# Optimization experiments

Measured on AMD Instinct MI355X. Metric: run time of the kernel, lower is better.

The kernel has to match this reference:

```python
import jax, jax.numpy as jnp
import numpy as np

T, B, E, H = 2048, 2, 1024, 16
HD = E // H
NEG = -1e9  # large negative for causal additive mask


def setup_inputs() -> dict:
    key = jax.random.key(0)
    ks = jax.random.split(key, 6)
    s = 0.02
    query = jax.random.normal(ks[0], (T, B, E), jnp.float32)
    # causal additive mask, as commonly passed to this module's attn_mask arg
    attn_mask = jnp.triu(jnp.full((T, T), NEG, jnp.float32), k=1)
    key_padding_mask = jnp.zeros((B, T), jnp.bool_)
    Wq = jax.random.normal(ks[1], (E, E), jnp.float32) * s
    Wk = jax.random.normal(ks[2], (E, E), jnp.float32) * s
    Wv = jax.random.normal(ks[3], (E, E), jnp.float32) * s
    Wo = jax.random.normal(ks[4], (E, E), jnp.float32) * s
    bq = jnp.zeros((E,), jnp.float32)
    bk = jnp.zeros((E,), jnp.float32)
    bv = jnp.zeros((E,), jnp.float32)
    bo = jnp.zeros((E,), jnp.float32)
    return {"query": query, "attn_mask": attn_mask, "key_padding_mask": key_padding_mask,
            "Wq": Wq, "bq": bq, "Wk": Wk, "bk": bk, "Wv": Wv, "bv": bv, "Wo": Wo, "bo": bo}


def _shape(x):
    # [T, B, E] -> [B*H, T, HD]; E splits as (H, HD), flat index = b*H + h
    return x.reshape(T, B * H, HD).transpose(1, 0, 2)


def reference(query, attn_mask, key_padding_mask, Wq, bq, Wk, bk, Wv, bv, Wo, bo):
    scaling = HD ** -0.5
    q = (query @ Wq.T + bq) * scaling  # scale q as in torch code
    k = query @ Wk.T + bk              # self-attention path (static_kv=False)
    v = query @ Wv.T + bv
    q, k, v = _shape(q), _shape(k), _shape(v)            # [B*H, T, HD]
    w = jnp.einsum('bth,bsh->bts', q, k)                  # [B*H, T, S]
    w = w.reshape(B, H, T, T) + attn_mask                 # additive mask broadcast
    w = jnp.where(key_padding_mask[:, None, None, :], -jnp.inf, w)
    p = jax.nn.softmax(w, axis=-1).reshape(B * H, T, T)   # dropout p=0 (eval)
    o = jnp.einsum('bts,bsh->bth', p, v)                  # [B*H, T, HD]
    o = o.transpose(1, 0, 2).reshape(T, B, E)
    return o @ Wo.T + bo
```

## Files before the change

kernel.cpp:

```cpp
#include <hip/hip_runtime.h>

#define Tt 2048
#define Bb 2
#define Ee 1024
#define Hh 16
#define HD 64
#define BH 32

typedef __attribute__((ext_vector_type(8))) short short8;
typedef __attribute__((ext_vector_type(8))) __bf16 bf16x8;
typedef __attribute__((ext_vector_type(4))) float floatx4;

#define OFF_X  0
#define OFF_WQ 4194304
#define OFF_WK 5242880
#define OFF_WV 6291456
#define OFF_WO 7340032
#define OFF_Q  8388608
#define OFF_K  12582912
#define OFF_V  16777216
#define OFF_O  20971520

__device__ __forceinline__ short f2bf(float f) {
  union { float f; unsigned u; } a; a.f = f;
  unsigned r = a.u + 0x7fffu + ((a.u >> 16) & 1u);
  return (short)(r >> 16);
}

__device__ __forceinline__ floatx4 mfma16(short8 a, short8 b, floatx4 c) {
  return __builtin_amdgcn_mfma_f32_16x16x32_bf16(
      __builtin_bit_cast(bf16x8, a), __builtin_bit_cast(bf16x8, b), c, 0, 0, 0);
}

__device__ __forceinline__ void gl_lds16(const short* g, short* l) {
  __builtin_amdgcn_global_load_lds(
      (const __attribute__((address_space(1))) void*)g,
      (__attribute__((address_space(3))) void*)l, 16, 0, 0);
}

__global__ __launch_bounds__(256)
void convert_kernel(const float* __restrict__ x, const float* __restrict__ wq,
                    const float* __restrict__ wk, const float* __restrict__ wv,
                    const float* __restrict__ wo, short* __restrict__ dst)
{
  const int i4 = blockIdx.x * 256 + threadIdx.x;
  const int f = i4 * 4;
  const float* src;
  int local;
  if (f < 4194304) { src = x; local = f; }
  else {
    int gg = f - 4194304;
    int wsel = gg >> 20;
    local = gg & 1048575;
    src = (wsel == 0) ? wq : (wsel == 1) ? wk : (wsel == 2) ? wv : wo;
  }
  floatx4 v = *reinterpret_cast<const floatx4*>(src + local);
  short4 o;
  o.x = f2bf(v[0]); o.y = f2bf(v[1]); o.z = f2bf(v[2]); o.w = f2bf(v[3]);
  *reinterpret_cast<short4*>(dst + f) = o;
}

__global__ __launch_bounds__(256)
void qkv_kernel(short* __restrict__ ws, const float* __restrict__ bq,
                const float* __restrict__ bk, const float* __restrict__ bv)
{
  __shared__ short As[64 * 64];
  __shared__ short Bs[192 * 64];
  const int t = threadIdx.x;
  const int lane = t & 63;
  const int w = t >> 6;
  const int g = lane >> 4, c = lane & 15;
  const int rb = blockIdx.x * 64;
  const int h = blockIdx.y;
  const int rw = (w >> 1) * 32, cw = (w & 1) * 96;

  const short* gA[2]; int oA[2];
#pragma unroll
  for (int i = 0; i < 2; i++) {
    const int cid = t + 256 * i;
    const int row = cid >> 3;
    const int col8 = (cid & 7) ^ (row & 7);
    gA[i] = ws + OFF_X + (rb + row) * 1024 + col8 * 8;
    oA[i] = cid * 8;
  }
  const short* gB[6]; int oB[6];
#pragma unroll
  for (int i = 0; i < 6; i++) {
    const int cid = t + 256 * i;
    const int row = cid >> 3;
    const int col8 = (cid & 7) ^ (row & 7);
    const short* wbase = ws + (row < 64 ? OFF_WQ : (row < 128 ? OFF_WK : OFF_WV));
    gB[i] = wbase + (h * 64 + (row & 63)) * 1024 + col8 * 8;
    oB[i] = cid * 8;
  }

  const int x0 = (g ^ (c & 7)) * 8;
  floatx4 acc[2][6];
#pragma unroll
  for (int i = 0; i < 2; i++)
#pragma unroll
    for (int j = 0; j < 6; j++) acc[i][j] = (floatx4){0.f, 0.f, 0.f, 0.f};

  for (int k0 = 0; k0 < 1024; k0 += 64) {
#pragma unroll
    for (int i = 0; i < 2; i++) gl_lds16(gA[i] + k0, As + oA[i]);
#pragma unroll
    for (int i = 0; i < 6; i++) gl_lds16(gB[i] + k0, Bs + oB[i]);
    __syncthreads();
#pragma unroll
    for (int kk = 0; kk < 2; kk++) {
      const int xo = x0 ^ (kk * 32);
      short8 af[2], bfr[6];
#pragma unroll
      for (int mi = 0; mi < 2; mi++)
        af[mi] = *reinterpret_cast<const short8*>(As + (rw + mi * 16 + c) * 64 + xo);
#pragma unroll
      for (int ni = 0; ni < 6; ni++)
        bfr[ni] = *reinterpret_cast<const short8*>(Bs + (cw + ni * 16 + c) * 64 + xo);
#pragma unroll
      for (int mi = 0; mi < 2; mi++)
#pragma unroll
        for (int ni = 0; ni < 6; ni++)
          acc[mi][ni] = mfma16(af[mi], bfr[ni], acc[mi][ni]);
    }
    __syncthreads();
  }

#pragma unroll
  for (int ni = 0; ni < 6; ni++) {
    const int gcol = cw + ni * 16;
    const int mat = gcol >> 6;
    if (mat < 2) {
      const int d = (gcol & 63) + c;
      const float bcol = (mat == 0 ? bq : bk)[h * 64 + d];
#pragma unroll
      for (int mi = 0; mi < 2; mi++)
#pragma unroll
        for (int r = 0; r < 4; r++) {
          const int row = rb + rw + mi * 16 + g * 4 + r;
          const int tt = row >> 1, b = row & 1;
          float v = acc[mi][ni][r] + bcol;
          if (mat == 0) v *= 0.18033688f;
          ws[(mat == 0 ? OFF_Q : OFF_K) + ((b * Hh + h) * Tt + tt) * HD + d] = f2bf(v);
        }
    }
  }
  for (int b = 0; b < 2; b++) {
#pragma unroll
    for (int ni = 2; ni < 6; ni++) {
      const int gcol = cw + ni * 16;
      if (gcol >= 128) {
        const int d = (gcol - 128) + c;
        const float bcol = bv[h * 64 + d];
#pragma unroll
        for (int mi = 0; mi < 2; mi++)
#pragma unroll
          for (int rr = 0; rr < 2; rr++) {
            const int r = rr * 2 + b;
            const int rloc = rw + mi * 16 + g * 4 + r;
            As[d * 40 + (rloc >> 1)] = f2bf(acc[mi][ni][r] + bcol);
          }
      }
    }
    __syncthreads();
    {
      const int d = t >> 2, seg = t & 3;
      short8 vv = *reinterpret_cast<const short8*>(As + d * 40 + seg * 8);
      *reinterpret_cast<short8*>(ws + OFF_V + ((b * Hh + h) * HD + d) * Tt
                                 + (rb >> 1) + seg * 8) = vv;
    }
    __syncthreads();
  }
}

__global__ __launch_bounds__(256)
void gemm_o(const short* __restrict__ ws, const float* __restrict__ bo,
            float* __restrict__ dout)
{
  __shared__ short As[64 * 64];
  __shared__ short Bs[64 * 64];
  const int t = threadIdx.x;
  const int lane = t & 63;
  const int w = t >> 6;
  const int g = lane >> 4, c = lane & 15;
  const int rb = blockIdx.x * 64, cb = blockIdx.y * 64;
  const int rw = (w >> 1) * 32, cw = (w & 1) * 32;

  const short* gA[2]; const short* gB[2]; int oo[2];
#pragma unroll
  for (int i = 0; i < 2; i++) {
    const int cid = t + 256 * i;
    const int row = cid >> 3;
    const int col8 = (cid & 7) ^ (row & 7);
    gA[i] = ws + OFF_O + (rb + row) * 1024 + col8 * 8;
    gB[i] = ws + OFF_WO + (cb + row) * 1024 + col8 * 8;
    oo[i] = cid * 8;
  }

  const int x0 = (g ^ (c & 7)) * 8;
  floatx4 acc[2][2];
#pragma unroll
  for (int i = 0; i < 2; i++)
#pragma unroll
    for (int j = 0; j < 2; j++) acc[i][j] = (floatx4){0.f, 0.f, 0.f, 0.f};

  for (int k0 = 0; k0 < 1024; k0 += 64) {
#pragma unroll
    for (int i = 0; i < 2; i++) gl_lds16(gA[i] + k0, As + oo[i]);
#pragma unroll
    for (int i = 0; i < 2; i++) gl_lds16(gB[i] + k0, Bs + oo[i]);
    __syncthreads();
#pragma unroll
    for (int kk = 0; kk < 2; kk++) {
      const int xo = x0 ^ (kk * 32);
      short8 af[2], bfr[2];
#pragma unroll
      for (int mi = 0; mi < 2; mi++)
        af[mi] = *reinterpret_cast<const short8*>(As + (rw + mi * 16 + c) * 64 + xo);
#pragma unroll
      for (int ni = 0; ni < 2; ni++)
        bfr[ni] = *reinterpret_cast<const short8*>(Bs + (cw + ni * 16 + c) * 64 + xo);
#pragma unroll
      for (int mi = 0; mi < 2; mi++)
#pragma unroll
        for (int ni = 0; ni < 2; ni++)
          acc[mi][ni] = mfma16(af[mi], bfr[ni], acc[mi][ni]);
    }
    __syncthreads();
  }

#pragma unroll
  for (int ni = 0; ni < 2; ni++) {
    const int col = cb + cw + ni * 16 + c;
    const float bcol = bo[col];
#pragma unroll
    for (int mi = 0; mi < 2; mi++)
#pragma unroll
      for (int r = 0; r < 4; r++) {
        const int row = rb + rw + mi * 16 + g * 4 + r;
        dout[row * 1024 + col] = acc[mi][ni][r] + bcol;
      }
  }
}

__global__ __launch_bounds__(256)
void attn_kernel(short* __restrict__ ws, const unsigned char* __restrict__ kpm)
{
  __shared__ short Ks[4096];
  __shared__ short Vs[4096];
  __shared__ short Ps[4][16][72];
  const int t = threadIdx.x;
  const int lane = t & 63;
  const int w = t >> 6;
  const int g = lane >> 4, c = lane & 15;
  const int bh = blockIdx.x;
  const int b = bh >> 4;
  const int h = bh & 15;
  const int qt = 31 - blockIdx.y;
  const int qrow0 = qt * 64;
  const int wrow = qrow0 + w * 16;

  const short* Qp = ws + OFF_Q + bh * Tt * HD;
  const short* Kp = ws + OFF_K + bh * Tt * HD;
  const short* Vp = ws + OFF_V + bh * HD * Tt;

  const short* gK[2]; const short* gV[2]; int lo[2];
#pragma unroll
  for (int i = 0; i < 2; i++) {
    const int cid = t + 256 * i;
    const int row = cid >> 3;
    const int col8 = (cid & 7) ^ (row & 7);
    gK[i] = Kp + row * HD + col8 * 8;
    gV[i] = Vp + row * Tt + col8 * 8;
    lo[i] = cid * 8;
  }
  const int x0 = (g ^ (c & 7)) * 8;

  const short8 aq0 = *reinterpret_cast<const short8*>(Qp + (wrow + c) * HD + g * 8);
  const short8 aq1 = *reinterpret_cast<const short8*>(Qp + (wrow + c) * HD + 32 + g * 8);

  const uint4* kpv = reinterpret_cast<const uint4*>(kpm + b * Tt);
  uint4 k0v = kpv[lane * 2], k1v = kpv[lane * 2 + 1];
  const bool nz = (k0v.x | k0v.y | k0v.z | k0v.w | k1v.x | k1v.y | k1v.z | k1v.w) != 0;
  const unsigned long long kpany = __ballot(nz);

  float lt = 0.f;
  floatx4 acc[4];
#pragma unroll
  for (int nt = 0; nt < 4; nt++) acc[nt] = (floatx4){0.f, 0.f, 0.f, 0.f};

  const int ktmax = qt;
  for (int kt = 0; kt <= ktmax; kt++) {
    const int k0 = kt * 64;
#pragma unroll
    for (int i = 0; i < 2; i++) gl_lds16(gK[i] + k0 * HD, &Ks[lo[i]]);
#pragma unroll
    for (int i = 0; i < 2; i++) gl_lds16(gV[i] + k0, &Vs[lo[i]]);
    __syncthreads();

    if (k0 <= wrow + 15) {
      floatx4 st[4];
#pragma unroll
      for (int nt = 0; nt < 4; nt++) {
        const short* kr = &Ks[(nt * 16 + c) * 64];
        short8 kb0 = *reinterpret_cast<const short8*>(kr + x0);
        short8 kb1 = *reinterpret_cast<const short8*>(kr + (x0 ^ 32));
        floatx4 z = (floatx4){0.f, 0.f, 0.f, 0.f};
        z = mfma16(kb0, aq0, z);
        z = mfma16(kb1, aq1, z);
        st[nt] = z;
      }
      if ((kpany >> (2 * kt)) & 3ULL) {
#pragma unroll
        for (int nt = 0; nt < 4; nt++)
#pragma unroll
          for (int r = 0; r < 4; r++)
            if (kpm[b * Tt + k0 + nt * 16 + g * 4 + r] != 0) st[nt][r] = -1e30f;
      }
      if (k0 + 63 > wrow) {
        const int trow = wrow + c;
#pragma unroll
        for (int nt = 0; nt < 4; nt++) {
          const int sbase = k0 + nt * 16 + g * 4;
#pragma unroll
          for (int r = 0; r < 4; r++)
            if (sbase + r > trow) st[nt][r] = -1e30f;
        }
      }
#pragma unroll
      for (int nt = 0; nt < 4; nt++) {
        float p0 = __builtin_amdgcn_exp2f(st[nt][0]);
        float p1 = __builtin_amdgcn_exp2f(st[nt][1]);
        float p2 = __builtin_amdgcn_exp2f(st[nt][2]);
        float p3 = __builtin_amdgcn_exp2f(st[nt][3]);
        lt += (p0 + p1) + (p2 + p3);
        unsigned u0 = __builtin_bit_cast(unsigned, p0) + 0x8000u;
        unsigned u1 = __builtin_bit_cast(unsigned, p1) + 0x8000u;
        unsigned u2 = __builtin_bit_cast(unsigned, p2) + 0x8000u;
        unsigned u3 = __builtin_bit_cast(unsigned, p3) + 0x8000u;
        uint2 pk;
        pk.x = __builtin_amdgcn_perm(u1, u0, 0x07060302u);
        pk.y = __builtin_amdgcn_perm(u3, u2, 0x07060302u);
        *reinterpret_cast<uint2*>(&Ps[w][c][nt * 16 + g * 4]) = pk;
      }
      const short8 pa0 = *reinterpret_cast<const short8*>(&Ps[w][c][g * 8]);
      const short8 pa1 = *reinterpret_cast<const short8*>(&Ps[w][c][32 + g * 8]);

#pragma unroll
      for (int nt = 0; nt < 4; nt++) {
        const short* vr = &Vs[(nt * 16 + c) * 64];
        short8 vb0 = *reinterpret_cast<const short8*>(vr + x0);
        short8 vb1 = *reinterpret_cast<const short8*>(vr + (x0 ^ 32));
        acc[nt] = mfma16(pa0, vb0, acc[nt]);
        acc[nt] = mfma16(pa1, vb1, acc[nt]);
      }
    }
    __syncthreads();
  }

  lt += __shfl_xor(lt, 16);
  lt += __shfl_xor(lt, 32);
  const float inv = 1.f / lt;
  float invr[4];
#pragma unroll
  for (int r = 0; r < 4; r++) invr[r] = __shfl(inv, g * 4 + r, 16);

#pragma unroll
  for (int nt = 0; nt < 4; nt++)
#pragma unroll
    for (int r = 0; r < 4; r++) {
      const int trow = wrow + g * 4 + r;
      const int col = h * 64 + nt * 16 + c;
      ws[OFF_O + (trow * Bb + b) * Ee + col] = f2bf(acc[nt][r] * invr[r]);
    }
}

extern "C" void kernel_launch(void* const* d_in, const int* in_sizes, int n_in,
                              void* d_out, int out_size, void* d_ws, size_t ws_size,
                              hipStream_t stream)
{
  const float* query = (const float*)d_in[0];
  const unsigned char* kpm = (const unsigned char*)d_in[2];
  const float* Wq = (const float*)d_in[3];
  const float* bq = (const float*)d_in[4];
  const float* Wk = (const float*)d_in[5];
  const float* bk = (const float*)d_in[6];
  const float* Wv = (const float*)d_in[7];
  const float* bv = (const float*)d_in[8];
  const float* Wo = (const float*)d_in[9];
  const float* bo = (const float*)d_in[10];
  short* ws = (short*)d_ws;
  float* out = (float*)d_out;

  convert_kernel<<<dim3(8192), dim3(256), 0, stream>>>(query, Wq, Wk, Wv, Wo, ws);
  qkv_kernel<<<dim3(64, 16), dim3(256), 0, stream>>>(ws, bq, bk, bv);
  attn_kernel<<<dim3(32, 32), dim3(256), 0, stream>>>(ws, kpm);
  gemm_o<<<dim3(64, 16), dim3(256), 0, stream>>>(ws, bo, out);
}
```

Baseline: 192.2 us.

## Retile QKV and output GEMMs to 128x128 with double-buffered LDS

Both projection GEMMs move from 64-wide tiles to 128x128 block tiles with a 64x64 tile per warp and a K step of 32. The K loop now double-buffers LDS, issuing the next tile's global-to-LDS loads before computing the current one, and uses one barrier per iteration. The QKV kernel treats Wq/Wk/Wv as one contiguous 3072-column matrix instead of one head per block, and rewrites its V-transpose epilogue to match. The goal is more data reuse per loaded byte and overlap of loads with MFMA work. The cost is fewer blocks (256 for the output GEMM) and higher register pressure from 16 accumulators.

After: 191.6 us. No clear change (-0.3%).

```diff
diff --git a/kernel.cpp b/kernel.cpp
--- a/kernel.cpp
+++ b/kernel.cpp
@@ -60,181 +60,189 @@
   *reinterpret_cast<short4*>(dst + f) = o;
 }
 
-__global__ __launch_bounds__(256)
+__global__ __launch_bounds__(256, 2)
 void qkv_kernel(short* __restrict__ ws, const float* __restrict__ bq,
                 const float* __restrict__ bk, const float* __restrict__ bv)
 {
-  __shared__ short As[64 * 64];
-  __shared__ short Bs[192 * 64];
+  __shared__ short smem[2][8192];
   const int t = threadIdx.x;
   const int lane = t & 63;
   const int w = t >> 6;
   const int g = lane >> 4, c = lane & 15;
-  const int rb = blockIdx.x * 64;
-  const int h = blockIdx.y;
-  const int rw = (w >> 1) * 32, cw = (w & 1) * 96;
-
-  const short* gA[2]; int oA[2];
+  const int rb = blockIdx.x * 128;
+  const int cb = blockIdx.y * 128;
+  const int rw = (w >> 1) * 64, cw2 = (w & 1) * 64;
+
+  const short* gA[2]; const short* gB[2]; int oC[2];
 #pragma unroll
   for (int i = 0; i < 2; i++) {
     const int cid = t + 256 * i;
-    const int row = cid >> 3;
-    const int col8 = (cid & 7) ^ (row & 7);
-    gA[i] = ws + OFF_X + (rb + row) * 1024 + col8 * 8;
-    oA[i] = cid * 8;
-  }
-  const short* gB[6]; int oB[6];
-#pragma unroll
-  for (int i = 0; i < 6; i++) {
-    const int cid = t + 256 * i;
-    const int row = cid >> 3;
-    const int col8 = (cid & 7) ^ (row & 7);
-    const short* wbase = ws + (row < 64 ? OFF_WQ : (row < 128 ? OFF_WK : OFF_WV));
-    gB[i] = wbase + (h * 64 + (row & 63)) * 1024 + col8 * 8;
-    oB[i] = cid * 8;
-  }
-
-  const int x0 = (g ^ (c & 7)) * 8;
-  floatx4 acc[2][6];
-#pragma unroll
-  for (int i = 0; i < 2; i++)
-#pragma unroll
-    for (int j = 0; j < 6; j++) acc[i][j] = (floatx4){0.f, 0.f, 0.f, 0.f};
-
-  for (int k0 = 0; k0 < 1024; k0 += 64) {
-#pragma unroll
-    for (int i = 0; i < 2; i++) gl_lds16(gA[i] + k0, As + oA[i]);
-#pragma unroll
-    for (int i = 0; i < 6; i++) gl_lds16(gB[i] + k0, Bs + oB[i]);
+    const int row = cid >> 2;
+    const int lch = (cid & 3) ^ ((row + (row >> 2)) & 3);
+    gA[i] = ws + OFF_X + (rb + row) * 1024 + lch * 8;
+    gB[i] = ws + OFF_WQ + (cb + row) * 1024 + lch * 8;
+    oC[i] = cid * 8;
+  }
+  const int xr = (g ^ ((c + (c >> 2)) & 3)) * 8;
+
+  floatx4 acc[4][4];
+#pragma unroll
+  for (int i = 0; i < 4; i++)
+#pragma unroll
+    for (int j = 0; j < 4; j++) acc[i][j] = (floatx4){0.f, 0.f, 0.f, 0.f};
+
+#pragma unroll
+  for (int i = 0; i < 2; i++) {
+    gl_lds16(gA[i], &smem[0][oC[i]]);
+    gl_lds16(gB[i], &smem[0][4096 + oC[i]]);
+  }
+  __syncthreads();
+
+  for (int kt = 0; kt < 32; kt++) {
+    const int cur = kt & 1;
+    if (kt < 31) {
+      const int kn = (kt + 1) * 32;
+#pragma unroll
+      for (int i = 0; i < 2; i++) {
+        gl_lds16(gA[i] + kn, &smem[cur ^ 1][oC[i]]);
+        gl_lds16(gB[i] + kn, &smem[cur ^ 1][4096 + oC[i]]);
+      }
+    }
+    short8 af[4], bf[4];
+#pragma unroll
+    for (int mi = 0; mi < 4; mi++)
+      af[mi] = *reinterpret_cast<const short8*>(&smem[cur][(rw + mi * 16 + c) * 32 + xr]);
+#pragma unroll
+    for (int ni = 0; ni < 4; ni++)
+      bf[ni] = *reinterpret_cast<const short8*>(&smem[cur][4096 + (cw2 + ni * 16 + c) * 32 + xr]);
+#pragma unroll
+    for (int mi = 0; mi < 4; mi++)
+#pragma unroll
+      for (int ni = 0; ni < 4; ni++)
+        acc[mi][ni] = mfma16(af[mi], bf[ni], acc[mi][ni]);
     __syncthreads();
-#pragma unroll
-    for (int kk = 0; kk < 2; kk++) {
-      const int xo = x0 ^ (kk * 32);
-      short8 af[2], bfr[6];
-#pragma unroll
-      for (int mi = 0; mi < 2; mi++)
-        af[mi] = *reinterpret_cast<const short8*>(As + (rw + mi * 16 + c) * 64 + xo);
-#pragma unroll
-      for (int ni = 0; ni < 6; ni++)
-        bfr[ni] = *reinterpret_cast<const short8*>(Bs + (cw + ni * 16 + c) * 64 + xo);
-#pragma unroll
-      for (int mi = 0; mi < 2; mi++)
-#pragma unroll
-        for (int ni = 0; ni < 6; ni++)
-          acc[mi][ni] = mfma16(af[mi], bfr[ni], acc[mi][ni]);
-    }
-    __syncthreads();
-  }
-
-#pragma unroll
-  for (int ni = 0; ni < 6; ni++) {
-    const int gcol = cw + ni * 16;
-    const int mat = gcol >> 6;
-    if (mat < 2) {
-      const int d = (gcol & 63) + c;
-      const float bcol = (mat == 0 ? bq : bk)[h * 64 + d];
-#pragma unroll
-      for (int mi = 0; mi < 2; mi++)
+  }
+
+  const int m = cb >> 10;
+  const int lcb = cb & 1023;
+  if (m < 2) {
+#pragma unroll
+    for (int ni = 0; ni < 4; ni++) {
+      const int lc = lcb + cw2 + ni * 16 + c;
+      const int h = lc >> 6, d = lc & 63;
+      const float bcol = (m == 0 ? bq : bk)[lc];
+#pragma unroll
+      for (int mi = 0; mi < 4; mi++)
 #pragma unroll
         for (int r = 0; r < 4; r++) {
           const int row = rb + rw + mi * 16 + g * 4 + r;
           const int tt = row >> 1, b = row & 1;
           float v = acc[mi][ni][r] + bcol;
-          if (mat == 0) v *= 0.18033688f;
-          ws[(mat == 0 ? OFF_Q : OFF_K) + ((b * Hh + h) * Tt + tt) * HD + d] = f2bf(v);
+          if (m == 0) v *= 0.18033688f;
+          ws[(m == 0 ? OFF_Q : OFF_K) + ((b * Hh + h) * Tt + tt) * HD + d] = f2bf(v);
         }
     }
-  }
-  for (int b = 0; b < 2; b++) {
-#pragma unroll
-    for (int ni = 2; ni < 6; ni++) {
-      const int gcol = cw + ni * 16;
-      if (gcol >= 128) {
-        const int d = (gcol - 128) + c;
-        const float bcol = bv[h * 64 + d];
-#pragma unroll
-        for (int mi = 0; mi < 2; mi++)
+  } else {
+    short* vt = &smem[0][0];
+    const int hb = lcb >> 6;
+    for (int b = 0; b < 2; b++) {
+      __syncthreads();
+#pragma unroll
+      for (int ni = 0; ni < 4; ni++) {
+        const int lcol = cw2 + ni * 16 + c;
+        const float bcol = bv[lcb + lcol];
+#pragma unroll
+        for (int mi = 0; mi < 4; mi++)
 #pragma unroll
           for (int rr = 0; rr < 2; rr++) {
             const int r = rr * 2 + b;
             const int rloc = rw + mi * 16 + g * 4 + r;
-            As[d * 40 + (rloc >> 1)] = f2bf(acc[mi][ni][r] + bcol);
+            vt[lcol * 72 + (rloc >> 1)] = f2bf(acc[mi][ni][r] + bcol);
           }
       }
-    }
-    __syncthreads();
-    {
-      const int d = t >> 2, seg = t & 3;
-      short8 vv = *reinterpret_cast<const short8*>(As + d * 40 + seg * 8);
-      *reinterpret_cast<short8*>(ws + OFF_V + ((b * Hh + h) * HD + d) * Tt
-                                 + (rb >> 1) + seg * 8) = vv;
-    }
-    __syncthreads();
-  }
-}
-
-__global__ __launch_bounds__(256)
+      __syncthreads();
+#pragma unroll
+      for (int i = 0; i < 4; i++) {
+        const int u = t + 256 * i;
+        const int lcol = u >> 3, seg = u & 7;
+        short8 vv = *reinterpret_cast<const short8*>(vt + lcol * 72 + seg * 8);
+        const int h = hb + (lcol >> 6), d = lcol & 63;
+        *reinterpret_cast<short8*>(ws + OFF_V + ((b * Hh + h) * HD + d) * Tt
+                                   + (rb >> 1) + seg * 8) = vv;
+      }
+    }
+  }
+}
+
+__global__ __launch_bounds__(256, 2)
 void gemm_o(const short* __restrict__ ws, const float* __restrict__ bo,
             float* __restrict__ dout)
 {
-  __shared__ short As[64 * 64];
-  __shared__ short Bs[64 * 64];
+  __shared__ short smem[2][8192];
   const int t = threadIdx.x;
   const int lane = t & 63;
   const int w = t >> 6;
   const int g = lane >> 4, c = lane & 15;
-  const int rb = blockIdx.x * 64, cb = blockIdx.y * 64;
-  const int rw = (w >> 1) * 32, cw = (w & 1) * 32;
-
-  const short* gA[2]; const short* gB[2]; int oo[2];
+  const int rb = blockIdx.x * 128;
+  const int cb = blockIdx.y * 128;
+  const int rw = (w >> 1) * 64, cw2 = (w & 1) * 64;
+
+  const short* gA[2]; const short* gB[2]; int oC[2];
 #pragma unroll
   for (int i = 0; i < 2; i++) {
     const int cid = t + 256 * i;
-    const int row = cid >> 3;
-    const int col8 = (cid & 7) ^ (row & 7);
-    gA[i] = ws + OFF_O + (rb + row) * 1024 + col8 * 8;
-    gB[i] = ws + OFF_WO + (cb + row) * 1024 + col8 * 8;
-    oo[i] = cid * 8;
-  }
-
-  const int x0 = (g ^ (c & 7)) * 8;
-  floatx4 acc[2][2];
-#pragma unroll
-  for (int i = 0; i < 2; i++)
-#pragma unroll
-    for (int j = 0; j < 2; j++) acc[i][j] = (floatx4){0.f, 0.f, 0.f, 0.f};
-
-  for (int k0 = 0; k0 < 1024; k0 += 64) {
-#pragma unroll
-    for (int i = 0; i < 2; i++) gl_lds16(gA[i] + k0, As + oo[i]);
-#pragma unroll
-    for (int i = 0; i < 2; i++) gl_lds16(gB[i] + k0, Bs + oo[i]);
+    const int row = cid >> 2;
+    const int lch = (cid & 3) ^ ((row + (row >> 2)) & 3);
+    gA[i] = ws + OFF_O + (rb + row) * 1024 + lch * 8;
+    gB[i] = ws + OFF_WO + (cb + row) * 1024 + lch * 8;
+    oC[i] = cid * 8;
+  }
+  const int xr = (g ^ ((c + (c >> 2)) & 3)) * 8;
+
+  floatx4 acc[4][4];
+#pragma unroll
+  for (int i = 0; i < 4; i++)
+#pragma unroll
+    for (int j = 0; j < 4; j++) acc[i][j] = (floatx4){0.f, 0.f, 0.f, 0.f};
+
+#pragma unroll
+  for (int i = 0; i < 2; i++) {
+    gl_lds16(gA[i], &smem[0][oC[i]]);
+    gl_lds16(gB[i], &smem[0][4096 + oC[i]]);
+  }
+  __syncthreads();
+
+  for (int kt = 0; kt < 32; kt++) {
+    const int cur = kt & 1;
+    if (kt < 31) {
+      const int kn = (kt + 1) * 32;
+#pragma unroll
+      for (int i = 0; i < 2; i++) {
+        gl_lds16(gA[i] + kn, &smem[cur ^ 1][oC[i]]);
+        gl_lds16(gB[i] + kn, &smem[cur ^ 1][4096 + oC[i]]);
+      }
+    }
+    short8 af[4], bf[4];
+#pragma unroll
+    for (int mi = 0; mi < 4; mi++)
+      af[mi] = *reinterpret_cast<const short8*>(&smem[cur][(rw + mi * 16 + c) * 32 + xr]);
+#pragma unroll
+    for (int ni = 0; ni < 4; ni++)
+      bf[ni] = *reinterpret_cast<const short8*>(&smem[cur][4096 + (cw2 + ni * 16 + c) * 32 + xr]);
+#pragma unroll
+    for (int mi = 0; mi < 4; mi++)
+#pragma unroll
+      for (int ni = 0; ni < 4; ni++)
+        acc[mi][ni] = mfma16(af[mi], bf[ni], acc[mi][ni]);
     __syncthreads();
-#pragma unroll
-    for (int kk = 0; kk < 2; kk++) {
-      const int xo = x0 ^ (kk * 32);
-      short8 af[2], bfr[2];
-#pragma unroll
-      for (int mi = 0; mi < 2; mi++)
-        af[mi] = *reinterpret_cast<const short8*>(As + (rw + mi * 16 + c) * 64 + xo);
-#pragma unroll
-      for (int ni = 0; ni < 2; ni++)
-        bfr[ni] = *reinterpret_cast<const short8*>(Bs + (cw + ni * 16 + c) * 64 + xo);
-#pragma unroll
-      for (int mi = 0; mi < 2; mi++)
-#pragma unroll
-        for (int ni = 0; ni < 2; ni++)
-          acc[mi][ni] = mfma16(af[mi], bfr[ni], acc[mi][ni]);
-    }
-    __syncthreads();
-  }
-
-#pragma unroll
-  for (int ni = 0; ni < 2; ni++) {
-    const int col = cb + cw + ni * 16 + c;
+  }
+
+#pragma unroll
+  for (int ni = 0; ni < 4; ni++) {
+    const int col = cb + cw2 + ni * 16 + c;
     const float bcol = bo[col];
 #pragma unroll
-    for (int mi = 0; mi < 2; mi++)
+    for (int mi = 0; mi < 4; mi++)
 #pragma unroll
       for (int r = 0; r < 4; r++) {
         const int row = rb + rw + mi * 16 + g * 4 + r;
@@ -393,7 +401,7 @@
   float* out = (float*)d_out;
 
   convert_kernel<<<dim3(8192), dim3(256), 0, stream>>>(query, Wq, Wk, Wv, Wo, ws);
-  qkv_kernel<<<dim3(64, 16), dim3(256), 0, stream>>>(ws, bq, bk, bv);
+  qkv_kernel<<<dim3(32, 24), dim3(256), 0, stream>>>(ws, bq, bk, bv);
   attn_kernel<<<dim3(32, 32), dim3(256), 0, stream>>>(ws, kpm);
-  gemm_o<<<dim3(64, 16), dim3(256), 0, stream>>>(ws, bo, out);
-}
+  gemm_o<<<dim3(32, 8), dim3(256), 0, stream>>>(ws, bo, out);
+}
```
